# Performance work log

Hardware: AMD Instinct MI355X
Metric: run time of the kernel (lower is better)

Reference implementation:

```python
import jax, jax.numpy as jnp
import numpy as np

N_Q = 8
DIM = 2 ** N_Q          # 256
DEGREE = 3
ANSATZ_LAYERS = 2


def gelu(x):
    return jax.nn.gelu(x, approximate=False)


def layer_norm(x, g, b, eps=1e-5):
    mu = x.mean(-1, keepdims=True)
    v = x.var(-1, keepdims=True)
    return (x - mu) / jnp.sqrt(v + eps) * g + b


def apply_ry(state, theta, w, n):
    # state: (B, 2^n) complex64, theta: (B,) per-element angle
    half = theta * 0.5
    c, s = jnp.cos(half), jnp.sin(half)
    U = jnp.stack([jnp.stack([c, -s], -1), jnp.stack([s, c], -1)], -2).astype(state.dtype)
    L, R = 2 ** w, 2 ** (n - 1 - w)
    st = state.reshape(-1, L, 2, R)
    st = jnp.einsum('bij,bljr->blir', U, st)
    return st.reshape(state.shape)


def apply_crx(state, theta, c, t, n):
    # controlled-RX(theta), control wire c, target wire t (batched angles)
    half = theta * 0.5
    cs = jnp.cos(half).astype(state.dtype)
    ms = (-1j) * jnp.sin(half).astype(state.dtype)
    Rx = jnp.stack([jnp.stack([cs, ms], -1), jnp.stack([ms, cs], -1)], -2)  # (B,2,2)
    a, b = min(c, t), max(c, t)
    A, M, R = 2 ** a, 2 ** (b - a - 1), 2 ** (n - 1 - b)
    st = state.reshape(-1, A, 2, M, 2, R)
    if c < t:
        sub = st[:, :, 1]                              # control bit = 1 slice, (B,A,M,2,R)
        sub = jnp.einsum('bij,bamjr->bamir', Rx, sub)
        st = st.at[:, :, 1].set(sub)
    else:
        sub = st[:, :, :, :, 1]                        # (B,A,2,M,R)
        sub = jnp.einsum('bij,bajmr->baimr', Rx, sub)
        st = st.at[:, :, :, :, 1].set(sub)
    return st.reshape(state.shape)


def sim14(state, params, n, layers):
    # Sim et al. 2019 circuit 14: RY layer, CRX ring, RY layer, reversed CRX ring (4n params/layer)
    idx = 0
    for _ in range(layers):
        for q in range(n):
            state = apply_ry(state, params[:, idx + q], q, n)
        idx += n
        for q in range(n):
            state = apply_crx(state, params[:, idx + q], q, (q + 1) % n, n)
        idx += n
        for q in range(n):
            state = apply_ry(state, params[:, idx + q], q, n)
        idx += n
        for q in range(n):
            state = apply_crx(state, params[:, idx + q], q, (q - 1) % n, n)
        idx += n
    return state


def pauli_expvals(psi, n):
    # [<X_0..X_{n-1}>, <Y_0..>, <Z_0..>] for batched pure states psi: (B, 2^n)
    xs, ys, zs = [], [], []
    for w in range(n):
        L, R = 2 ** w, 2 ** (n - 1 - w)
        s = psi.reshape(-1, L, 2, R)
        s0, s1 = s[:, :, 0], s[:, :, 1]
        cross = (jnp.conj(s0) * s1).sum((1, 2))
        xs.append(2.0 * jnp.real(cross))
        ys.append(2.0 * jnp.imag(cross))
        zs.append((jnp.abs(s0) ** 2 - jnp.abs(s1) ** 2).sum((1, 2)))
    return jnp.stack(xs + ys + zs, axis=1).astype(jnp.float32)


def dwsep_conv(x, dw_w, dw_b, pw_w, pw_b, gn_g, gn_b, dilation):
    # depthwise-separable conv1d + GroupNorm(8) + GELU; x: (B, C, T)
    k = dw_w.shape[-1]
    pad = (k - 1) * dilation // 2
    y = jax.lax.conv_general_dilated(
        x, dw_w, window_strides=(1,), padding=[(pad, pad)], rhs_dilation=(dilation,),
        feature_group_count=x.shape[1], dimension_numbers=('NCH', 'OIH', 'NCH'))
    y = y + dw_b[None, :, None]
    y = jnp.einsum('oc,bct->bot', pw_w, y) + pw_b[None, :, None]
    B, C, T = y.shape
    g = y.reshape(B, 8, C // 8, T)
    mu = g.mean((2, 3), keepdims=True)
    var = g.var((2, 3), keepdims=True)
    y = ((g - mu) / jnp.sqrt(var + 1e-5)).reshape(B, C, T)
    return gelu(y * gn_g[None, :, None] + gn_b[None, :, None])


def setup_inputs() -> dict:
    key = jax.random.key(0)
    ks = iter(jax.random.split(key, 64))
    rn = lambda *s: jax.random.normal(next(ks), s, jnp.float32) * 0.05
    ru = lambda *s: jax.random.uniform(next(ks), s, dtype=jnp.float32)
    inp = dict(
        x=jax.random.normal(next(ks), (16, 363, 180), jnp.float32),
        net_w=rn(12, 15, 8), net_b=rn(12, 8),
        dwa_w=rn(96, 1, 7), dwa_b=rn(96), pwa_w=rn(96, 96), pwa_b=rn(96),
        gna_g=jnp.ones(96, jnp.float32), gna_b=jnp.zeros(96, jnp.float32),
        dwb_w=rn(96, 1, 7), dwb_b=rn(96), pwb_w=rn(96, 96), pwb_b=rn(96),
        gnb_g=jnp.ones(96, jnp.float32), gnb_b=jnp.zeros(96, jnp.float32),
        dwc_w=rn(96, 1, 7), dwc_b=rn(96), pwc_w=rn(96, 96), pwc_b=rn(96),
        gnc_g=jnp.ones(96, jnp.float32), gnc_b=jnp.zeros(96, jnp.float32),
        merge_w=rn(288, 128), merge_b=rn(128),
        merge_ln_g=jnp.ones(128, jnp.float32), merge_ln_b=jnp.zeros(128, jnp.float32),
        qproj_w=rn(128, 64), qproj_b=rn(64),
        poly_coeffs=ru(4), qff_params=ru(32),
        mix_re=ru(363), mix_im=ru(363),
        qout_w=rn(24, 128), qout_b=rn(128),
        fc_w=rn(78, 64), fc_b=rn(64),
        fus1_w=rn(192, 128), fus1_b=rn(128),
        fus_ln_g=jnp.ones(128, jnp.float32), fus_ln_b=jnp.zeros(128, jnp.float32),
        fus2_w=rn(128, 64), fus2_b=rn(64),
    )
    return inp


def reference(x, net_w, net_b, dwa_w, dwa_b, pwa_w, pwa_b, gna_g, gna_b,
              dwb_w, dwb_b, pwb_w, pwb_b, gnb_g, gnb_b,
              dwc_w, dwc_b, pwc_w, pwc_b, gnc_g, gnc_b,
              merge_w, merge_b, merge_ln_g, merge_ln_b,
              qproj_w, qproj_b, poly_coeffs, qff_params, mix_re, mix_im,
              qout_w, qout_b, fc_w, fc_b,
              fus1_w, fus1_b, fus_ln_g, fus_ln_b, fus2_w, fus2_b):
    B, T, C = x.shape
    # --- network projection: 12 contiguous networks of 15 ROIs -> d_net=8 each ---
    h = jnp.einsum('btki,kid->btkd', x.reshape(B, T, 12, 15), net_w) + net_b
    h = gelu(h).reshape(B, T, 96)
    # --- multiscale depthwise-separable convs ---
    ht = h.transpose(0, 2, 1)  # (B,96,T)
    a = dwsep_conv(ht, dwa_w, dwa_b, pwa_w, pwa_b, gna_g, gna_b, 1)
    b = dwsep_conv(ht, dwb_w, dwb_b, pwb_w, pwb_b, gnb_g, gnb_b, 4)
    c = dwsep_conv(ht, dwc_w, dwc_b, pwc_w, pwc_b, gnc_g, gnc_b, 16)
    cat = jnp.concatenate([a, b, c], axis=1).transpose(0, 2, 1)  # (B,T,288)
    h = gelu(layer_norm(cat @ merge_w + merge_b, merge_ln_g, merge_ln_b))  # (B,T,128)
    # --- QSVT quantum temporal mixing ---
    tp = jax.nn.sigmoid(h @ qproj_w + qproj_b) * (2.0 * np.pi)  # (B,T,64) rotation angles
    tp = tp.reshape(B * T, -1)
    base = jnp.zeros((B * T, DIM), jnp.complex64).at[:, 0].set(1.0)
    pc = poly_coeffs.astype(jnp.complex64)
    state = base
    acc = pc[0] * base
    for d in range(1, DEGREE + 1):
        state = sim14(state, tp, N_Q, ANSATZ_LAYERS)
        acc = acc + pc[d] * state
    acc = acc.reshape(B, T, DIM)
    mix = (mix_re + 1j * mix_im).astype(jnp.complex64)[:T]
    mixed = jnp.einsum('t,btd->bd', mix, acc)           # temporal mixing
    norm = jnp.linalg.norm(mixed, axis=1, keepdims=True)
    psi = mixed / (norm + 1e-9)
    psi = sim14(psi, jnp.broadcast_to(qff_params[None, :], (B, qff_params.shape[0])), N_Q, 1)
    exps = pauli_expvals(psi, N_Q)                      # (B,24)
    temporal = exps @ qout_w + qout_b                   # (B,128)
    # --- FC fingerprint ---
    xm = x - x.mean(1, keepdims=True)
    std = jnp.maximum(jnp.std(x, axis=1, keepdims=True, ddof=1), 1e-8)
    xn = xm / std
    corr = jnp.einsum('btc,btd->bcd', xn, xn) / (T - 1)
    bm = corr.reshape(B, 12, 15, 12, 15).mean((2, 4))   # (B,12,12) network-block means
    iu0, iu1 = jnp.triu_indices(12)
    fc_vec = bm[:, iu0, iu1]                            # (B,78)
    fc = gelu(fc_vec @ fc_w + fc_b)                     # (B,64)
    # --- fusion ---
    fused = jnp.concatenate([temporal, fc], axis=1)
    out = gelu(layer_norm(fused @ fus1_w + fus1_b, fus_ln_g, fus_ln_b)) @ fus2_w + fus2_b
    return out  # (B,64)
```

## Files before the change

kernel.cpp:

```cpp
#include <hip/hip_runtime.h>
#include <math.h>

#define NB 16
#define NT 363
#define NC 180
#define SZF 557568
#define NROW 5808

__device__ __forceinline__ float gelu_f(float x) {
  return 0.5f * x * (1.0f + erff(x * 0.7071067811865475244f));
}


template<int CTRL>
__device__ __forceinline__ float dppf(float x) {
  return __int_as_float(__builtin_amdgcn_update_dpp(
      0, __float_as_int(x), CTRL, 0xF, 0xF, true));
}

template<int LB>
__device__ __forceinline__ float lx(float x) {
  if constexpr (LB == 0) return dppf<0xB1>(x);
  else if constexpr (LB == 1) return dppf<0x4E>(x);
  else if constexpr (LB == 2) return __shfl_xor(x, 4);
  else return __shfl_xor(x, 8);
}

template<int P>
__device__ __forceinline__ void ry_local(float* re, float* im, float c, float s) {
#pragma unroll
  for (int j = 0; j < 16; ++j) {
    if ((j & (1 << P)) == 0) {
      int k = j | (1 << P);
      float r0 = re[j], i0 = im[j], r1 = re[k], i1 = im[k];
      re[j] = fmaf(c, r0, -s * r1); im[j] = fmaf(c, i0, -s * i1);
      re[k] = fmaf(s, r0,  c * r1); im[k] = fmaf(s, i0,  c * i1);
    }
  }
}

template<int LB>
__device__ __forceinline__ void ry_lane(float* re, float* im, float c, float s, int lane) {
  float sg = (lane & (1 << LB)) ? s : -s;
#pragma unroll
  for (int j = 0; j < 16; ++j) {
    float br = lx<LB>(re[j]);
    float bi = lx<LB>(im[j]);
    re[j] = fmaf(c, re[j], sg * br);
    im[j] = fmaf(c, im[j], sg * bi);
  }
}

template<int Q, int P>
__device__ __forceinline__ void crx_ll(float* re, float* im, float cs, float sn) {
#pragma unroll
  for (int j = 0; j < 16; ++j) {
    if ((j & (1 << Q)) && !(j & (1 << P))) {
      int k = j | (1 << P);
      float r0 = re[j], i0 = im[j], r1 = re[k], i1 = im[k];
      re[j] = fmaf(cs, r0,  sn * i1); im[j] = fmaf(cs, i0, -sn * r1);
      re[k] = fmaf(cs, r1,  sn * i0); im[k] = fmaf(cs, i1, -sn * r0);
    }
  }
}

template<int LBQ, int P>
__device__ __forceinline__ void crx_nl(float* re, float* im, float cs, float sn, int lane) {
  if (lane & (1 << LBQ)) {
#pragma unroll
    for (int j = 0; j < 16; ++j) {
      if ((j & (1 << P)) == 0) {
        int k = j | (1 << P);
        float r0 = re[j], i0 = im[j], r1 = re[k], i1 = im[k];
        re[j] = fmaf(cs, r0,  sn * i1); im[j] = fmaf(cs, i0, -sn * r1);
        re[k] = fmaf(cs, r1,  sn * i0); im[k] = fmaf(cs, i1, -sn * r0);
      }
    }
  }
}

template<int Q, int LBP>
__device__ __forceinline__ void crx_ln(float* re, float* im, float cs, float sn) {
#pragma unroll
  for (int j = 0; j < 16; ++j) {
    if (j & (1 << Q)) {
      float br = lx<LBP>(re[j]);
      float bi = lx<LBP>(im[j]);
      re[j] = fmaf(cs, re[j],  sn * bi);
      im[j] = fmaf(cs, im[j], -sn * br);
    }
  }
}

template<int LBQ, int LBP>
__device__ __forceinline__ void crx_nn(float* re, float* im, float cs, float sn, int lane) {
  bool ctl = (lane & (1 << LBQ)) != 0;
#pragma unroll
  for (int j = 0; j < 16; ++j) {
    float br = lx<LBP>(re[j]);
    float bi = lx<LBP>(im[j]);
    if (ctl) {
      re[j] = fmaf(cs, re[j],  sn * bi);
      im[j] = fmaf(cs, im[j], -sn * br);
    }
  }
}

__device__ __forceinline__ void qlayer(float* re, float* im,
                                       const float2* ang, int lane) {
  float2 a;
  a = ang[0];  ry_lane<3>(re, im, a.x, a.y, lane);
  a = ang[1];  ry_lane<2>(re, im, a.x, a.y, lane);
  a = ang[2];  ry_lane<1>(re, im, a.x, a.y, lane);
  a = ang[3];  ry_lane<0>(re, im, a.x, a.y, lane);
  a = ang[4];  ry_local<3>(re, im, a.x, a.y);
  a = ang[5];  ry_local<2>(re, im, a.x, a.y);
  a = ang[6];  ry_local<1>(re, im, a.x, a.y);
  a = ang[7];  ry_local<0>(re, im, a.x, a.y);
  a = ang[8];  crx_nn<3, 2>(re, im, a.x, a.y, lane);
  a = ang[9];  crx_nn<2, 1>(re, im, a.x, a.y, lane);
  a = ang[10]; crx_nn<1, 0>(re, im, a.x, a.y, lane);
  a = ang[11]; crx_nl<0, 3>(re, im, a.x, a.y, lane);
  a = ang[12]; crx_ll<3, 2>(re, im, a.x, a.y);
  a = ang[13]; crx_ll<2, 1>(re, im, a.x, a.y);
  a = ang[14]; crx_ll<1, 0>(re, im, a.x, a.y);
  a = ang[15]; crx_ln<0, 3>(re, im, a.x, a.y);
  a = ang[16]; ry_lane<3>(re, im, a.x, a.y, lane);
  a = ang[17]; ry_lane<2>(re, im, a.x, a.y, lane);
  a = ang[18]; ry_lane<1>(re, im, a.x, a.y, lane);
  a = ang[19]; ry_lane<0>(re, im, a.x, a.y, lane);
  a = ang[20]; ry_local<3>(re, im, a.x, a.y);
  a = ang[21]; ry_local<2>(re, im, a.x, a.y);
  a = ang[22]; ry_local<1>(re, im, a.x, a.y);
  a = ang[23]; ry_local<0>(re, im, a.x, a.y);
  a = ang[24]; crx_nl<3, 0>(re, im, a.x, a.y, lane);
  a = ang[25]; crx_nn<2, 3>(re, im, a.x, a.y, lane);
  a = ang[26]; crx_nn<1, 2>(re, im, a.x, a.y, lane);
  a = ang[27]; crx_nn<0, 1>(re, im, a.x, a.y, lane);
  a = ang[28]; crx_ln<3, 0>(re, im, a.x, a.y);
  a = ang[29]; crx_ll<2, 3>(re, im, a.x, a.y);
  a = ang[30]; crx_ll<1, 2>(re, im, a.x, a.y);
  a = ang[31]; crx_ll<0, 1>(re, im, a.x, a.y);
}

template<int P>
__device__ __forceinline__ void ryg(float* re, float* im, float c, float s, int lane) {
  if constexpr (P >= 2) {
    constexpr int mask = 1 << (P - 2);
    float sg = ((lane >> (P - 2)) & 1) ? s : -s;
#pragma unroll
    for (int j = 0; j < 4; ++j) {
      float br = __shfl_xor(re[j], mask);
      float bi = __shfl_xor(im[j], mask);
      re[j] = fmaf(c, re[j], sg * br);
      im[j] = fmaf(c, im[j], sg * bi);
    }
  } else {
#pragma unroll
    for (int k = 0; k < 2; ++k) {
      const int a = (P == 0) ? 2 * k : k;
      const int b = (P == 0) ? a + 1 : a + 2;
      float r0 = re[a], i0 = im[a], r1 = re[b], i1 = im[b];
      re[a] = fmaf(c, r0, -s * r1); im[a] = fmaf(c, i0, -s * i1);
      re[b] = fmaf(s, r0,  c * r1); im[b] = fmaf(s, i0,  c * i1);
    }
  }
}

template<int PC, int PT>
__device__ __forceinline__ void crxg(float* re, float* im, float cs, float sn, int lane) {
  if constexpr (PT >= 2) {
    constexpr int mask = 1 << (PT - 2);
#pragma unroll
    for (int j = 0; j < 4; ++j) {
      float br = __shfl_xor(re[j], mask);
// ... 6 lines not shown
        float ni = fmaf(cs, im[j], -sn * br);
        re[j] = nr; im[j] = ni;
      }
    }
  } else {
#pragma unroll
    for (int k = 0; k < 2; ++k) {
      const int a = (PT == 0) ? 2 * k : k;
      const int b = (PT == 0) ? a + 1 : a + 2;
      bool ctrl;
      if constexpr (PC >= 2) ctrl = ((lane >> (PC - 2)) & 1) != 0;
      else                   ctrl = ((a >> PC) & 1) != 0;
      if (ctrl) {
        float r0 = re[a], i0 = im[a], r1 = re[b], i1 = im[b];
        re[a] = fmaf(cs, r0,  sn * i1); im[a] = fmaf(cs, i0, -sn * r1);
        re[b] = fmaf(cs, r1,  sn * i0); im[b] = fmaf(cs, i1, -sn * r0);
      }
    }
  }
}

__device__ __forceinline__ void sim14_layer(float* re, float* im,
                                            const float* Cr, const float* Sr, int lane) {
#define ARY1(q, pi) ryg<7-(q)>(re, im, Cr[pi], Sr[pi], lane)
#define ACX1(cq, tq, pi) crxg<7-(cq), 7-(tq)>(re, im, Cr[pi], Sr[pi], lane)
  ARY1(0,0); ARY1(1,1); ARY1(2,2); ARY1(3,3); ARY1(4,4); ARY1(5,5); ARY1(6,6); ARY1(7,7);
  ACX1(0,1,8); ACX1(1,2,9); ACX1(2,3,10); ACX1(3,4,11); ACX1(4,5,12); ACX1(5,6,13); ACX1(6,7,14); ACX1(7,0,15);
  ARY1(0,16); ARY1(1,17); ARY1(2,18); ARY1(3,19); ARY1(4,20); ARY1(5,21); ARY1(6,22); ARY1(7,23);
  ACX1(0,7,24); ACX1(1,0,25); ACX1(2,1,26); ACX1(3,2,27); ACX1(4,3,28); ACX1(5,4,29); ACX1(6,5,30); ACX1(7,6,31);
#undef ARY1
#undef ACX1
}

__global__ __launch_bounds__(256) void k_embed(const float* __restrict__ x,
                                               const float* __restrict__ nw,
                                               const float* __restrict__ nb,
                                               float* __restrict__ ht) {
  int b = blockIdx.x, tile = blockIdx.y, tid = threadIdx.x;
  int t0 = tile * 32;
  __shared__ float xt[32][181];
  __shared__ float nwL[1440];
  __shared__ float nbL[96];
  for (int i = tid; i < 1440; i += 256) nwL[i] = nw[i];
  for (int i = tid; i < 96; i += 256) nbL[i] = nb[i];
  for (int i = tid; i < 32 * 180; i += 256) {
    int tt = i / 180, c = i % 180;
    int t = t0 + tt;
    xt[tt][c] = (t < NT) ? x[(b * NT + t) * NC + c] : 0.0f;
  }
  __syncthreads();
  int tt = tid & 31, cs = tid >> 5;
  int t = t0 + tt;
  if (t < NT) {
    for (int pass = 0; pass < 12; ++pass) {
      int k = pass, d = cs;
      int c = k * 8 + d;
      float acc = nbL[k * 8 + d];
#pragma unroll
      for (int i = 0; i < 15; ++i)
        acc = fmaf(xt[tt][k * 15 + i], nwL[(k * 15 + i) * 8 + d], acc);
      ht[(b * 96 + c) * NT + t] = gelu_f(acc);
    }
  }
}

__global__ __launch_bounds__(384) void k_dw(const float* __restrict__ ht,
    const float* __restrict__ wa, const float* __restrict__ ba,
    const float* __restrict__ wb, const float* __restrict__ bb,
    const float* __restrict__ wc, const float* __restrict__ bc,
    float* __restrict__ y1base) {
  int bc_idx = blockIdx.x;
  int c = bc_idx % 96;
  int tid = threadIdx.x;
  __shared__ float rowL[NT];
  if (tid < NT) rowL[tid] = ht[bc_idx * NT + tid];
  __syncthreads();
  if (tid < NT) {
    {
      float acc = ba[c];
#pragma unroll
      for (int k = 0; k < 7; ++k) {
        int idx = tid + (k - 3);
        if (idx >= 0 && idx < NT) acc = fmaf(rowL[idx], wa[c * 7 + k], acc);
      }
      y1base[bc_idx * NT + tid] = acc;
    }
    {
      float acc = bb[c];
#pragma unroll
      for (int k = 0; k < 7; ++k) {
        int idx = tid + (k - 3) * 4;
        if (idx >= 0 && idx < NT) acc = fmaf(rowL[idx], wb[c * 7 + k], acc);
      }
      y1base[SZF + bc_idx * NT + tid] = acc;
    }
    {
      float acc = bc[c];
#pragma unroll
      for (int k = 0; k < 7; ++k) {
        int idx = tid + (k - 3) * 16;
        if (idx >= 0 && idx < NT) acc = fmaf(rowL[idx], wc[c * 7 + k], acc);
      }
      y1base[2 * SZF + bc_idx * NT + tid] = acc;
    }
  }
}

__global__ __launch_bounds__(256) void k_pw(const float* __restrict__ y1base,
    const float* __restrict__ wA, const float* __restrict__ wB, const float* __restrict__ wC,
    const float* __restrict__ bA, const float* __restrict__ bB, const float* __restrict__ bC,
    float* __restrict__ y2base) {
  int b = blockIdx.x, tile = blockIdx.y, z = blockIdx.z, tid = threadIdx.x;
  const float* pw_w = (z == 0) ? wA : ((z == 1) ? wB : wC);
  const float* pw_b = (z == 0) ? bA : ((z == 1) ? bB : bC);
  const float* y1 = y1base + (size_t)z * SZF;
  float* y2 = y2base + (size_t)z * SZF;
  int t0 = tile * 64;
  __shared__ float y1t[96 * 64];
  __shared__ float pwL[96 * 97];
  for (int i = tid; i < 96 * 96; i += 256) {
    int o = i / 96, cc = i % 96;
    pwL[o * 97 + cc] = pw_w[i];
  }
  for (int i = tid; i < 96 * 64; i += 256) {
    int cc = i >> 6, t = i & 63;
    int tt = t0 + t;
    y1t[i] = (tt < NT) ? y1[(b * 96 + cc) * NT + tt] : 0.0f;
  }
  __syncthreads();
  int o16 = tid >> 4, t4 = (tid & 15) * 4;
  for (int pass = 0; pass < 6; ++pass) {
    int o = pass * 16 + o16;
    float bias = pw_b[o];
    float a0 = bias, a1 = bias, a2 = bias, a3 = bias;
    const float* wrow = &pwL[o * 97];
#pragma unroll 4
    for (int cc = 0; cc < 96; ++cc) {
// ... 95 lines not shown
  for (int r = 0; r < 4; ++r) vL[rg * 4 + r][jj] = acc[r];
  __syncthreads();
  if (tid < 8) {
    float s = 0;
    for (int k = 0; k < 128; ++k) s += vL[tid][k];
    float mu = s / 128.0f;
    float q = 0;
    for (int k = 0; k < 128; ++k) { float d = vL[tid][k] - mu; q = fmaf(d, d, q); }
    muS[tid] = mu;
    rsS[tid] = rsqrtf(q / 128.0f + 1e-5f);
  }
  __syncthreads();
  float g = lng[jj], bb2 = lnb[jj];
#pragma unroll
  for (int r = 0; r < 4; ++r) {
    int row = rg * 4 + r;
    float h = (acc[r] - muS[row]) * rsS[row] * g + bb2;
    hL[row][jj] = gelu_f(h);
  }
  __syncthreads();
  int o = tid & 63;
  int r0 = (tid >> 6) * 2;
  for (int rr = 0; rr < 2; ++rr) {
    int row = r0 + rr;
    float u = qb[o];
    for (int k = 0; k < 128; ++k) u = fmaf(hL[row][k], qw[k * 64 + o], u);
    float tp = 6.2831853071795864769f / (1.0f + expf(-u));
    float hf = tp * 0.5f;
    int grow = blk * 8 + row;
    angG[grow * 64 + o] = make_float2(cosf(hf), sinf(hf));
  }
}

__global__ __launch_bounds__(64) void k_quantum(const float2* __restrict__ angG,
                                                const float* __restrict__ pc4,
                                                float* __restrict__ accG) {
  const int lane = threadIdx.x;
  const int g = lane >> 4;
  const int ll = lane & 15;
  const int row0 = blockIdx.x * 4;
  __shared__ float2 angL[4][66];
#pragma unroll
  for (int q = 0; q < 4; ++q)
    angL[q][lane] = angG[(size_t)(row0 + q) * 64 + lane];
  __syncthreads();
  float p0 = pc4[0], p1 = pc4[1], p2 = pc4[2], p3 = pc4[3];
  float re[16], im[16];
#pragma unroll
  for (int j = 0; j < 16; ++j) { re[j] = 0.0f; im[j] = 0.0f; }
  if (ll == 0) re[0] = p3;
  const float2* ang = &angL[g][0];
  for (int rep = 0; rep < 3; ++rep) {
    qlayer(re, im, ang, lane);
    qlayer(re, im, ang + 32, lane);
    float pc = (rep == 0) ? p2 : (rep == 1) ? p1 : p0;
    if (ll == 0) re[0] += pc;
  }
  int row = row0 + g;
  float4* dst = reinterpret_cast<float4*>(accG + ((size_t)row * 256 + ll * 16) * 2);
#pragma unroll
  for (int h = 0; h < 8; ++h)
    dst[h] = make_float4(re[2 * h], im[2 * h], re[2 * h + 1], im[2 * h + 1]);
}

__global__ __launch_bounds__(256) void k_mix1(const float* __restrict__ accG,
                                              const float* __restrict__ mr,
                                              const float* __restrict__ mi,
                                              float* __restrict__ part) {
  int b = blockIdx.x, ch = blockIdx.y, d = threadIdx.x;
  int t0 = ch * 33;
  float sr = 0, si = 0;
  for (int i = 0; i < 33; ++i) {
    int t = t0 + i;
    const float2 a = *reinterpret_cast<const float2*>(accG + (size_t)((b * NT + t) * 256 + d) * 2);
    float m_r = mr[t], m_i = mi[t];
    sr = fmaf(m_r, a.x, fmaf(-m_i, a.y, sr));
    si = fmaf(m_r, a.y, fmaf(m_i, a.x, si));
  }
  float2* o = reinterpret_cast<float2*>(part + (size_t)((b * 11 + ch) * 256 + d) * 2);
  *o = make_float2(sr, si);
}

__global__ __launch_bounds__(256) void k_tail(const float* __restrict__ part,
    const float* __restrict__ qff,
    const float* __restrict__ qout_w, const float* __restrict__ qout_b,
    const float* __restrict__ x,
    const float* __restrict__ fcw, const float* __restrict__ fcb,
    float* __restrict__ fused) {
  int blk = blockIdx.x, tid = threadIdx.x;
  if (blk < 16) {
    int b = blk;
    __shared__ float psiL[256][2];
    __shared__ float red[256];
    __shared__ float qcL[32], qsL[32], exps[24];
    float sr = 0, si = 0;
    {
      int d = tid;
      for (int ch = 0; ch < 11; ++ch) {
        const float2 a = *reinterpret_cast<const float2*>(part + (size_t)((b * 11 + ch) * 256 + d) * 2);
        sr += a.x; si += a.y;
      }
      psiL[d][0] = sr; psiL[d][1] = si;
      red[tid] = sr * sr + si * si;
    }
    if (tid < 32) { float h = qff[tid] * 0.5f; qcL[tid] = cosf(h); qsL[tid] = sinf(h); }
    __syncthreads();
    for (int s2 = 128; s2 > 0; s2 >>= 1) { if (tid < s2) red[tid] += red[tid + s2]; __syncthreads(); }
    float inv = 1.0f / (sqrtf(red[0]) + 1e-9f);
    __syncthreads();
    if (tid < 64) {
      int lane = tid;
      float re[4], im[4];
#pragma unroll
      for (int j = 0; j < 4; ++j) {
        re[j] = psiL[lane * 4 + j][0] * inv;
        im[j] = psiL[lane * 4 + j][1] * inv;
      }
      sim14_layer(re, im, qcL, qsL, lane);
#pragma unroll
      for (int j = 0; j < 4; ++j) { psiL[lane * 4 + j][0] = re[j]; psiL[lane * 4 + j][1] = im[j]; }
    }
    __syncthreads();
    if (tid < 64) {
      int lane = tid;
      for (int w = 0; w < 8; ++w) {
        int p = 7 - w;
        float cr = 0, ci = 0, z = 0;
#pragma unroll
        for (int k = 0; k < 2; ++k) {
          int pr = lane + k * 64;
          int lowmask = (1 << p) - 1;
          int i0 = ((pr >> p) << (p + 1)) | (pr & lowmask);
          int i1 = i0 | (1 << p);
          float r0 = psiL[i0][0], I0 = psiL[i0][1], r1 = psiL[i1][0], I1 = psiL[i1][1];
          cr += r0 * r1 + I0 * I1;
          ci += r0 * I1 - I0 * r1;
          z += r0 * r0 + I0 * I0 - r1 * r1 - I1 * I1;
        }
        for (int off = 32; off > 0; off >>= 1) {
          cr += __shfl_down(cr, off);
          ci += __shfl_down(ci, off);
          z  += __shfl_down(z, off);
        }
        if (lane == 0) { exps[w] = 2.0f * cr; exps[8 + w] = 2.0f * ci; exps[16 + w] = z; }
      }
    }
    __syncthreads();
    if (tid < 128) {
      float v = qout_b[tid];
#pragma unroll
      for (int k = 0; k < 24; ++k) v = fmaf(exps[k], qout_w[k * 128 + tid], v);
      fused[b * 192 + tid] = v;
    }
  } else {
    int b = blk - 16;
    __shared__ float muL[180], invL[180];
    __shared__ float SL[NT * 12];
    __shared__ float fcv[78];
    if (tid < 180) {
      float s = 0;
      const float* px = x + (size_t)b * NT * NC + tid;
      for (int t = 0; t < NT; ++t) s += px[t * NC];
      float mu = s / 363.0f;
      float q = 0;
      for (int t = 0; t < NT; ++t) { float d = px[t * NC] - mu; q = fmaf(d, d, q); }
      float sd = sqrtf(q / 362.0f);
      sd = fmaxf(sd, 1e-8f);
      muL[tid] = mu; invL[tid] = 1.0f / sd;
    }
    __syncthreads();
    for (int t = tid; t < NT; t += 256) {
      const float* px = x + (size_t)(b * NT + t) * NC;
#pragma unroll
      for (int i = 0; i < 12; ++i) {
        float s = 0;
#pragma unroll
        for (int u = 0; u < 15; ++u) {
          int cidx = i * 15 + u;
          s += (px[cidx] - muL[cidx]) * invL[cidx];
        }
        SL[t * 12 + i] = s;
      }
    }
    __syncthreads();
    if (tid < 78) {
      int i = 0, rem = tid;
      while (rem >= 12 - i) { rem -= 12 - i; ++i; }
      int j = i + rem;
      float acc = 0;
      for (int t = 0; t < NT; ++t) acc = fmaf(SL[t * 12 + i], SL[t * 12 + j], acc);
      fcv[tid] = acc * (1.0f / (225.0f * 362.0f));
    }
    __syncthreads();
    if (tid < 64) {
      float v = fcb[tid];
#pragma unroll
      for (int k = 0; k < 78; ++k) v = fmaf(fcv[k], fcw[k * 64 + tid], v);
      fused[b * 192 + 128 + tid] = gelu_f(v);
    }
  }
}

__global__ __launch_bounds__(128) void k_final(const float* __restrict__ fused,
    const float* __restrict__ w1, const float* __restrict__ b1,
    const float* __restrict__ lng, const float* __restrict__ lnb,
    const float* __restrict__ w2, const float* __restrict__ b2,
    float* __restrict__ out) {
  int b = blockIdx.x, tid = threadIdx.x;
  __shared__ float fL[192], red[128], hL[128];
  for (int i = tid; i < 192; i += 128) fL[i] = fused[b * 192 + i];
  __syncthreads();
  float v = b1[tid];
  for (int k = 0; k < 192; ++k) v = fmaf(fL[k], w1[k * 128 + tid], v);
  red[tid] = v; __syncthreads();
  for (int s = 64; s > 0; s >>= 1) { if (tid < s) red[tid] += red[tid + s]; __syncthreads(); }
  float mu = red[0] / 128.0f; __syncthreads();
  float dv = v - mu;
  red[tid] = dv * dv; __syncthreads();
  for (int s = 64; s > 0; s >>= 1) { if (tid < s) red[tid] += red[tid + s]; __syncthreads(); }
  float var = red[0] / 128.0f;
  float h = gelu_f(dv * rsqrtf(var + 1e-5f) * lng[tid] + lnb[tid]);
  hL[tid] = h; __syncthreads();
  if (tid < 64) {
    float o = b2[tid];
    for (int k = 0; k < 128; ++k) o = fmaf(hL[k], w2[k * 64 + tid], o);
    out[b * 64 + tid] = o;
  }
}

extern "C" void kernel_launch(void* const* d_in, const int* in_sizes, int n_in,
                              void* d_out, int out_size, void* d_ws, size_t ws_size,
                              hipStream_t stream) {
  const float* x       = (const float*)d_in[0];
  const float* net_w   = (const float*)d_in[1];
  const float* net_b   = (const float*)d_in[2];
  const float* dwa_w   = (const float*)d_in[3];
  const float* dwa_b   = (const float*)d_in[4];
  const float* pwa_w   = (const float*)d_in[5];
  const float* pwa_b   = (const float*)d_in[6];
  const float* gna_g   = (const float*)d_in[7];
  const float* gna_b   = (const float*)d_in[8];
  const float* dwb_w   = (const float*)d_in[9];
  const float* dwb_b   = (const float*)d_in[10];
  const float* pwb_w   = (const float*)d_in[11];
  const float* pwb_b   = (const float*)d_in[12];
  const float* gnb_g   = (const float*)d_in[13];
  const float* gnb_b   = (const float*)d_in[14];
  const float* dwc_w   = (const float*)d_in[15];
  const float* dwc_b   = (const float*)d_in[16];
  const float* pwc_w   = (const float*)d_in[17];
  const float* pwc_b   = (const float*)d_in[18];
  const float* gnc_g   = (const float*)d_in[19];
  const float* gnc_b   = (const float*)d_in[20];
  const float* merge_w = (const float*)d_in[21];
  const float* merge_b = (const float*)d_in[22];
  const float* mlng    = (const float*)d_in[23];
  const float* mlnb    = (const float*)d_in[24];
  const float* qproj_w = (const float*)d_in[25];
  const float* qproj_b = (const float*)d_in[26];
  const float* poly    = (const float*)d_in[27];
  const float* qff     = (const float*)d_in[28];
  const float* mix_re  = (const float*)d_in[29];
  const float* mix_im  = (const float*)d_in[30];
  const float* qout_w  = (const float*)d_in[31];
  const float* qout_b  = (const float*)d_in[32];
  const float* fc_w    = (const float*)d_in[33];
  const float* fc_b    = (const float*)d_in[34];
  const float* fus1_w  = (const float*)d_in[35];
  const float* fus1_b  = (const float*)d_in[36];
  const float* flng    = (const float*)d_in[37];
  const float* flnb    = (const float*)d_in[38];
  const float* fus2_w  = (const float*)d_in[39];
  const float* fus2_b  = (const float*)d_in[40];
  float* out = (float*)d_out;

  float* W = (float*)d_ws;
  float* ht    = W + 0;
  float* y1b_  = W + SZF;
  float* cat   = W + SZF;
  float* y2b_  = W + 4 * (size_t)SZF;
  float* acc   = W + 0;
  float2* angG = (float2*)(W + 7 * (size_t)SZF);
  float* muG   = W + 7 * (size_t)SZF + 743424;
  float* rsG   = muG + 512;
  float* part  = rsG + 512;
  float* fused = part + 90112;

  k_embed<<<dim3(NB, 12), 256, 0, stream>>>(x, net_w, net_b, ht);
  k_dw<<<NB * 96, 384, 0, stream>>>(ht, dwa_w, dwa_b, dwb_w, dwb_b, dwc_w, dwc_b, y1b_);
  k_pw<<<dim3(NB, 6, 3), 256, 0, stream>>>(y1b_, pwa_w, pwb_w, pwc_w, pwa_b, pwb_b, pwc_b, y2b_);
  k_gnstat<<<dim3(NB, 8, 3), 256, 0, stream>>>(y2b_, muG, rsG);
  k_gnapply<<<dim3(NB, 6, 3), 256, 0, stream>>>(y2b_, muG, rsG,
      gna_g, gnb_g, gnc_g, gna_b, gnb_b, gnc_b, cat);
  k_merge<<<(NB * NT) / 8, 256, 0, stream>>>(cat, merge_w, merge_b, mlng, mlnb,
                                             qproj_w, qproj_b, angG);
  k_quantum<<<NROW / 4, 64, 0, stream>>>(angG, poly, acc);
  k_mix1<<<dim3(NB, 11), 256, 0, stream>>>(acc, mix_re, mix_im, part);
  k_tail<<<32, 256, 0, stream>>>(part, qff, qout_w, qout_b, x, fc_w, fc_b, fused);
  k_final<<<NB, 128, 0, stream>>>(fused, fus1_w, fus1_b, flng, flnb, fus2_w, fus2_b, out);
}
```

Baseline: 337.7 us.

## Fuse embed with depthwise convs, repartition quantum state, merge tail kernels

```diff
diff --git a/kernel.cpp b/kernel.cpp
--- a/kernel.cpp
+++ b/kernel.cpp
@@ -23,13 +23,14 @@
   if constexpr (LB == 0) return dppf<0xB1>(x);
   else if constexpr (LB == 1) return dppf<0x4E>(x);
   else if constexpr (LB == 2) return __shfl_xor(x, 4);
-  else return __shfl_xor(x, 8);
+  else if constexpr (LB == 3) return __shfl_xor(x, 8);
+  else return __shfl_xor(x, 16);
 }
 
 template<int P>
-__device__ __forceinline__ void ry_local(float* re, float* im, float c, float s) {
-#pragma unroll
-  for (int j = 0; j < 16; ++j) {
+__device__ __forceinline__ void ry_local8(float* re, float* im, float c, float s) {
+#pragma unroll
+  for (int j = 0; j < 8; ++j) {
     if ((j & (1 << P)) == 0) {
       int k = j | (1 << P);
       float r0 = re[j], i0 = im[j], r1 = re[k], i1 = im[k];
@@ -40,10 +41,10 @@
 }
 
 template<int LB>
-__device__ __forceinline__ void ry_lane(float* re, float* im, float c, float s, int lane) {
+__device__ __forceinline__ void ry_lane8(float* re, float* im, float c, float s, int lane) {
   float sg = (lane & (1 << LB)) ? s : -s;
 #pragma unroll
-  for (int j = 0; j < 16; ++j) {
+  for (int j = 0; j < 8; ++j) {
     float br = lx<LB>(re[j]);
     float bi = lx<LB>(im[j]);
     re[j] = fmaf(c, re[j], sg * br);
@@ -52,9 +53,9 @@
 }
 
 template<int Q, int P>
-__device__ __forceinline__ void crx_ll(float* re, float* im, float cs, float sn) {
-#pragma unroll
-  for (int j = 0; j < 16; ++j) {
+__device__ __forceinline__ void crx_ll8(float* re, float* im, float cs, float sn) {
+#pragma unroll
+  for (int j = 0; j < 8; ++j) {
     if ((j & (1 << Q)) && !(j & (1 << P))) {
       int k = j | (1 << P);
       float r0 = re[j], i0 = im[j], r1 = re[k], i1 = im[k];
@@ -65,10 +66,10 @@
 }
 
 template<int LBQ, int P>
-__device__ __forceinline__ void crx_nl(float* re, float* im, float cs, float sn, int lane) {
+__device__ __forceinline__ void crx_nl8(float* re, float* im, float cs, float sn, int lane) {
   if (lane & (1 << LBQ)) {
 #pragma unroll
-    for (int j = 0; j < 16; ++j) {
+    for (int j = 0; j < 8; ++j) {
       if ((j & (1 << P)) == 0) {
         int k = j | (1 << P);
         float r0 = re[j], i0 = im[j], r1 = re[k], i1 = im[k];
@@ -80,9 +81,9 @@
 }
 
 template<int Q, int LBP>
-__device__ __forceinline__ void crx_ln(float* re, float* im, float cs, float sn) {
-#pragma unroll
-  for (int j = 0; j < 16; ++j) {
+__device__ __forceinline__ void crx_ln8(float* re, float* im, float cs, float sn) {
+#pragma unroll
+  for (int j = 0; j < 8; ++j) {
     if (j & (1 << Q)) {
       float br = lx<LBP>(re[j]);
       float bi = lx<LBP>(im[j]);
@@ -93,10 +94,10 @@
 }
 
 template<int LBQ, int LBP>
-__device__ __forceinline__ void crx_nn(float* re, float* im, float cs, float sn, int lane) {
+__device__ __forceinline__ void crx_nn8(float* re, float* im, float cs, float sn, int lane) {
   bool ctl = (lane & (1 << LBQ)) != 0;
 #pragma unroll
-  for (int j = 0; j < 16; ++j) {
+  for (int j = 0; j < 8; ++j) {
     float br = lx<LBP>(re[j]);
     float bi = lx<LBP>(im[j]);
     if (ctl) {
@@ -106,41 +107,41 @@
   }
 }
 
-__device__ __forceinline__ void qlayer(float* re, float* im,
-                                       const float2* ang, int lane) {
+__device__ __forceinline__ void qlayer8(float* re, float* im,
+                                        const float2* ang, int lane) {
   float2 a;
-  a = ang[0];  ry_lane<3>(re, im, a.x, a.y, lane);
-  a = ang[1];  ry_lane<2>(re, im, a.x, a.y, lane);
-  a = ang[2];  ry_lane<1>(re, im, a.x, a.y, lane);
-  a = ang[3];  ry_lane<0>(re, im, a.x, a.y, lane);
-  a = ang[4];  ry_local<3>(re, im, a.x, a.y);
-  a = ang[5];  ry_local<2>(re, im, a.x, a.y);
-  a = ang[6];  ry_local<1>(re, im, a.x, a.y);
-  a = ang[7];  ry_local<0>(re, im, a.x, a.y);
-  a = ang[8];  crx_nn<3, 2>(re, im, a.x, a.y, lane);
-  a = ang[9];  crx_nn<2, 1>(re, im, a.x, a.y, lane);
-  a = ang[10]; crx_nn<1, 0>(re, im, a.x, a.y, lane);
-  a = ang[11]; crx_nl<0, 3>(re, im, a.x, a.y, lane);
-  a = ang[12]; crx_ll<3, 2>(re, im, a.x, a.y);
-  a = ang[13]; crx_ll<2, 1>(re, im, a.x, a.y);
-  a = ang[14]; crx_ll<1, 0>(re, im, a.x, a.y);
-  a = ang[15]; crx_ln<0, 3>(re, im, a.x, a.y);
-  a = ang[16]; ry_lane<3>(re, im, a.x, a.y, lane);
-  a = ang[17]; ry_lane<2>(re, im, a.x, a.y, lane);
-  a = ang[18]; ry_lane<1>(re, im, a.x, a.y, lane);
-  a = ang[19]; ry_lane<0>(re, im, a.x, a.y, lane);
-  a = ang[20]; ry_local<3>(re, im, a.x, a.y);
-  a = ang[21]; ry_local<2>(re, im, a.x, a.y);
-  a = ang[22]; ry_local<1>(re, im, a.x, a.y);
-  a = ang[23]; ry_local<0>(re, im, a.x, a.y);
-  a = ang[24]; crx_nl<3, 0>(re, im, a.x, a.y, lane);
-  a = ang[25]; crx_nn<2, 3>(re, im, a.x, a.y, lane);
-  a = ang[26]; crx_nn<1, 2>(re, im, a.x, a.y, lane);
-  a = ang[27]; crx_nn<0, 1>(re, im, a.x, a.y, lane);
-  a = ang[28]; crx_ln<3, 0>(re, im, a.x, a.y);
-  a = ang[29]; crx_ll<2, 3>(re, im, a.x, a.y);
-  a = ang[30]; crx_ll<1, 2>(re, im, a.x, a.y);
-  a = ang[31]; crx_ll<0, 1>(re, im, a.x, a.y);
+  a = ang[0];  ry_lane8<4>(re, im, a.x, a.y, lane);
+  a = ang[1];  ry_lane8<3>(re, im, a.x, a.y, lane);
+  a = ang[2];  ry_lane8<2>(re, im, a.x, a.y, lane);
+  a = ang[3];  ry_lane8<1>(re, im, a.x, a.y, lane);
+  a = ang[4];  ry_lane8<0>(re, im, a.x, a.y, lane);
+  a = ang[5];  ry_local8<2>(re, im, a.x, a.y);
+  a = ang[6];  ry_local8<1>(re, im, a.x, a.y);
+  a = ang[7];  ry_local8<0>(re, im, a.x, a.y);
+  a = ang[8];  crx_nn8<4, 3>(re, im, a.x, a.y, lane);
+  a = ang[9];  crx_nn8<3, 2>(re, im, a.x, a.y, lane);
+  a = ang[10]; crx_nn8<2, 1>(re, im, a.x, a.y, lane);
+  a = ang[11]; crx_nn8<1, 0>(re, im, a.x, a.y, lane);
+  a = ang[12]; crx_nl8<0, 2>(re, im, a.x, a.y, lane);
+  a = ang[13]; crx_ll8<2, 1>(re, im, a.x, a.y);
+  a = ang[14]; crx_ll8<1, 0>(re, im, a.x, a.y);
+  a = ang[15]; crx_ln8<0, 4>(re, im, a.x, a.y);
+  a = ang[16]; ry_lane8<4>(re, im, a.x, a.y, lane);
+  a = ang[17]; ry_lane8<3>(re, im, a.x, a.y, lane);
+  a = ang[18]; ry_lane8<2>(re, im, a.x, a.y, lane);
+  a = ang[19]; ry_lane8<1>(re, im, a.x, a.y, lane);
+  a = ang[20]; ry_lane8<0>(re, im, a.x, a.y, lane);
+  a = ang[21]; ry_local8<2>(re, im, a.x, a.y);
+  a = ang[22]; ry_local8<1>(re, im, a.x, a.y);
+  a = ang[23]; ry_local8<0>(re, im, a.x, a.y);
+  a = ang[24]; crx_nl8<4, 0>(re, im, a.x, a.y, lane);
+  a = ang[25]; crx_nn8<3, 4>(re, im, a.x, a.y, lane);
+  a = ang[26]; crx_nn8<2, 3>(re, im, a.x, a.y, lane);
+  a = ang[27]; crx_nn8<1, 2>(re, im, a.x, a.y, lane);
+  a = ang[28]; crx_nn8<0, 1>(re, im, a.x, a.y, lane);
+  a = ang[29]; crx_ln8<2, 0>(re, im, a.x, a.y);
+  a = ang[30]; crx_ll8<1, 2>(re, im, a.x, a.y);
+  a = ang[31]; crx_ll8<0, 1>(re, im, a.x, a.y);
 }
 
 template<int P>
@@ -213,77 +214,60 @@
 #undef ACX1
 }
 
-__global__ __launch_bounds__(256) void k_embed(const float* __restrict__ x,
-                                               const float* __restrict__ nw,
-                                               const float* __restrict__ nb,
-                                               float* __restrict__ ht) {
-  int b = blockIdx.x, tile = blockIdx.y, tid = threadIdx.x;
-  int t0 = tile * 32;
-  __shared__ float xt[32][181];
-  __shared__ float nwL[1440];
-  __shared__ float nbL[96];
-  for (int i = tid; i < 1440; i += 256) nwL[i] = nw[i];
-  for (int i = tid; i < 96; i += 256) nbL[i] = nb[i];
-  for (int i = tid; i < 32 * 180; i += 256) {
-    int tt = i / 180, c = i % 180;
-    int t = t0 + tt;
-    xt[tt][c] = (t < NT) ? x[(b * NT + t) * NC + c] : 0.0f;
-  }
-  __syncthreads();
-  int tt = tid & 31, cs = tid >> 5;
-  int t = t0 + tt;
-  if (t < NT) {
-    for (int pass = 0; pass < 12; ++pass) {
-      int k = pass, d = cs;
-      int c = k * 8 + d;
-      float acc = nbL[k * 8 + d];
-#pragma unroll
-      for (int i = 0; i < 15; ++i)
-        acc = fmaf(xt[tt][k * 15 + i], nwL[(k * 15 + i) * 8 + d], acc);
-      ht[(b * 96 + c) * NT + t] = gelu_f(acc);
-    }
-  }
-}
-
-__global__ __launch_bounds__(384) void k_dw(const float* __restrict__ ht,
+__global__ __launch_bounds__(256) void k_emdw(const float* __restrict__ x,
+    const float* __restrict__ nw, const float* __restrict__ nb,
     const float* __restrict__ wa, const float* __restrict__ ba,
     const float* __restrict__ wb, const float* __restrict__ bb,
     const float* __restrict__ wc, const float* __restrict__ bc,
     float* __restrict__ y1base) {
-  int bc_idx = blockIdx.x;
-  int c = bc_idx % 96;
-  int tid = threadIdx.x;
-  __shared__ float rowL[NT];
-  if (tid < NT) rowL[tid] = ht[bc_idx * NT + tid];
-  __syncthreads();
-  if (tid < NT) {
-    {
-      float acc = ba[c];
-#pragma unroll
-      for (int k = 0; k < 7; ++k) {
-        int idx = tid + (k - 3);
-        if (idx >= 0 && idx < NT) acc = fmaf(rowL[idx], wa[c * 7 + k], acc);
-      }
-      y1base[bc_idx * NT + tid] = acc;
-    }
-    {
-      float acc = bb[c];
-#pragma unroll
-      for (int k = 0; k < 7; ++k) {
-        int idx = tid + (k - 3) * 4;
-        if (idx >= 0 && idx < NT) acc = fmaf(rowL[idx], wb[c * 7 + k], acc);
-      }
-      y1base[SZF + bc_idx * NT + tid] = acc;
-    }
-    {
-      float acc = bc[c];
-#pragma unroll
-      for (int k = 0; k < 7; ++k) {
-        int idx = tid + (k - 3) * 16;
-        if (idx >= 0 && idx < NT) acc = fmaf(rowL[idx], wc[c * 7 + k], acc);
-      }
-      y1base[2 * SZF + bc_idx * NT + tid] = acc;
-    }
+  int b = blockIdx.x, kg = blockIdx.y, tid = threadIdx.x;
+  __shared__ float xs[NT * 15];
+  __shared__ float nwL[120], nbL[8];
+  __shared__ float hrow[8][368];
+  __shared__ float wL[3][8][8];
+  __shared__ float bL[3][8];
+  for (int i = tid; i < 120; i += 256) nwL[i] = nw[kg * 120 + i];
+  for (int i = tid; i < 8; i += 256) nbL[i] = nb[kg * 8 + i];
+  for (int i = tid; i < 168; i += 256) {
+    int z = i / 56, r = i % 56, d = r / 7, k = r % 7;
+    const float* w = (z == 0) ? wa : ((z == 1) ? wb : wc);
+    wL[z][d][k] = w[(kg * 8 + d) * 7 + k];
+  }
+  for (int i = tid; i < 24; i += 256) {
+    int z = i / 8, d = i % 8;
+    const float* bias = (z == 0) ? ba : ((z == 1) ? bb : bc);
+    bL[z][d] = bias[kg * 8 + d];
+  }
+  for (int i = tid; i < NT * 15; i += 256) {
+    int t = i / 15, u = i % 15;
+    xs[i] = x[((size_t)b * NT + t) * NC + kg * 15 + u];
+  }
+  __syncthreads();
+  for (int i = tid; i < 8 * NT; i += 256) {
+    int t = i % NT, d = i / NT;
+    float acc2 = nbL[d];
+#pragma unroll
+    for (int u = 0; u < 15; ++u) acc2 = fmaf(xs[t * 15 + u], nwL[u * 8 + d], acc2);
+    hrow[d][t] = gelu_f(acc2);
+  }
+  __syncthreads();
+  for (int i = tid; i < 8 * NT; i += 256) {
+    int t = i % NT, d = i / NT;
+    int c = kg * 8 + d;
+    float a0 = bL[0][d], a1 = bL[1][d], a2 = bL[2][d];
+#pragma unroll
+    for (int k = 0; k < 7; ++k) {
+      int i1 = t + (k - 3);
+      int i4 = t + (k - 3) * 4;
+      int i16 = t + (k - 3) * 16;
+      if (i1 >= 0 && i1 < NT)  a0 = fmaf(hrow[d][i1],  wL[0][d][k], a0);
+      if (i4 >= 0 && i4 < NT)  a1 = fmaf(hrow[d][i4],  wL[1][d][k], a1);
+      if (i16 >= 0 && i16 < NT) a2 = fmaf(hrow[d][i16], wL[2][d][k], a2);
+    }
+    size_t base = ((size_t)b * 96 + c) * NT + t;
+    y1base[base] = a0;
+    y1base[SZF + base] = a1;
+    y1base[2 * SZF + base] = a2;
   }
 }
 
@@ -445,35 +429,90 @@
   }
 }
 
-__global__ __launch_bounds__(64) void k_quantum(const float2* __restrict__ angG,
-                                                const float* __restrict__ pc4,
-                                                float* __restrict__ accG) {
-  const int lane = threadIdx.x;
-  const int g = lane >> 4;
-  const int ll = lane & 15;
-  const int row0 = blockIdx.x * 4;
-  __shared__ float2 angL[4][66];
-#pragma unroll
-  for (int q = 0; q < 4; ++q)
-    angL[q][lane] = angG[(size_t)(row0 + q) * 64 + lane];
-  __syncthreads();
-  float p0 = pc4[0], p1 = pc4[1], p2 = pc4[2], p3 = pc4[3];
-  float re[16], im[16];
-#pragma unroll
-  for (int j = 0; j < 16; ++j) { re[j] = 0.0f; im[j] = 0.0f; }
-  if (ll == 0) re[0] = p3;
-  const float2* ang = &angL[g][0];
-  for (int rep = 0; rep < 3; ++rep) {
-    qlayer(re, im, ang, lane);
-    qlayer(re, im, ang + 32, lane);
-    float pc = (rep == 0) ? p2 : (rep == 1) ? p1 : p0;
-    if (ll == 0) re[0] += pc;
-  }
-  int row = row0 + g;
-  float4* dst = reinterpret_cast<float4*>(accG + ((size_t)row * 256 + ll * 16) * 2);
-#pragma unroll
-  for (int h = 0; h < 8; ++h)
-    dst[h] = make_float4(re[2 * h], im[2 * h], re[2 * h + 1], im[2 * h + 1]);
+struct CorrSM { float mu[180]; float inv[180]; float S[NT * 12]; float fcv[78]; };
+union QSM { float2 ang[8][66]; CorrSM c; };
+
+__global__ __launch_bounds__(256) void k_quantum(const float2* __restrict__ angG,
+                                                 const float* __restrict__ pc4,
+                                                 float* __restrict__ accG,
+                                                 const float* __restrict__ x,
+                                                 const float* __restrict__ fcw,
+                                                 const float* __restrict__ fcb,
+                                                 float* __restrict__ fusedG) {
+  __shared__ QSM sm;
+  int tid = threadIdx.x;
+  if (blockIdx.x < NROW / 8) {
+    const int lane = tid & 63;
+    const int wave = tid >> 6;
+    const int ll = lane & 31;
+    const int rowB = wave * 2 + (lane >> 5);
+    const int row0 = blockIdx.x * 8;
+    for (int i = tid; i < 512; i += 256) {
+      int r = i >> 6, cidx = i & 63;
+      sm.ang[r][cidx] = angG[(size_t)(row0 + r) * 64 + cidx];
+    }
+    __syncthreads();
+    float p0 = pc4[0], p1 = pc4[1], p2 = pc4[2], p3 = pc4[3];
+    float re[8], im[8];
+#pragma unroll
+    for (int j = 0; j < 8; ++j) { re[j] = 0.0f; im[j] = 0.0f; }
+    if (ll == 0) re[0] = p3;
+    const float2* ang = &sm.ang[rowB][0];
+    for (int rep = 0; rep < 3; ++rep) {
+      qlayer8(re, im, ang, lane);
+      qlayer8(re, im, ang + 32, lane);
+      float pc = (rep == 0) ? p2 : (rep == 1) ? p1 : p0;
+      if (ll == 0) re[0] += pc;
+    }
+    int row = row0 + rowB;
+    float4* dst = reinterpret_cast<float4*>(accG + ((size_t)row * 256 + ll * 8) * 2);
+#pragma unroll
+    for (int h = 0; h < 4; ++h)
+      dst[h] = make_float4(re[2 * h], im[2 * h], re[2 * h + 1], im[2 * h + 1]);
+  } else {
+    int b = blockIdx.x - NROW / 8;
+    if (tid < 180) {
+      float s = 0;
+      const float* px = x + (size_t)b * NT * NC + tid;
+      for (int t = 0; t < NT; ++t) s += px[t * NC];
+      float mu = s / 363.0f;
+      float q = 0;
+      for (int t = 0; t < NT; ++t) { float d = px[t * NC] - mu; q = fmaf(d, d, q); }
+      float sd = sqrtf(q / 362.0f);
+      sd = fmaxf(sd, 1e-8f);
+      sm.c.mu[tid] = mu; sm.c.inv[tid] = 1.0f / sd;
+    }
+    __syncthreads();
+    for (int t = tid; t < NT; t += 256) {
+      const float* px = x + (size_t)(b * NT + t) * NC;
+#pragma unroll
+      for (int i = 0; i < 12; ++i) {
+        float s = 0;
+#pragma unroll
+        for (int u = 0; u < 15; ++u) {
+          int cidx = i * 15 + u;
+          s += (px[cidx] - sm.c.mu[cidx]) * sm.c.inv[cidx];
+        }
+        sm.c.S[t * 12 + i] = s;
+      }
+    }
+    __syncthreads();
+    if (tid < 78) {
+      int i = 0, rem = tid;
+      while (rem >= 12 - i) { rem -= 12 - i; ++i; }
+      int j = i + rem;
+      float acc = 0;
+      for (int t = 0; t < NT; ++t) acc = fmaf(sm.c.S[t * 12 + i], sm.c.S[t * 12 + j], acc);
+      sm.c.fcv[tid] = acc * (1.0f / (225.0f * 362.0f));
+    }
+    __syncthreads();
+    if (tid < 64) {
+      float v = fcb[tid];
+#pragma unroll
+      for (int k = 0; k < 78; ++k) v = fmaf(sm.c.fcv[k], fcw[k * 64 + tid], v);
+      fusedG[b * 192 + 128 + tid] = gelu_f(v);
+    }
+  }
 }
 
 __global__ __launch_bounds__(256) void k_mix1(const float* __restrict__ accG,
@@ -497,143 +536,95 @@
 __global__ __launch_bounds__(256) void k_tail(const float* __restrict__ part,
     const float* __restrict__ qff,
     const float* __restrict__ qout_w, const float* __restrict__ qout_b,
-    const float* __restrict__ x,
-    const float* __restrict__ fcw, const float* __restrict__ fcb,
-    float* __restrict__ fused) {
-  int blk = blockIdx.x, tid = threadIdx.x;
-  if (blk < 16) {
-    int b = blk;
-    __shared__ float psiL[256][2];
-    __shared__ float red[256];
-    __shared__ float qcL[32], qsL[32], exps[24];
-    float sr = 0, si = 0;
-    {
-      int d = tid;
-      for (int ch = 0; ch < 11; ++ch) {
-        const float2 a = *reinterpret_cast<const float2*>(part + (size_t)((b * 11 + ch) * 256 + d) * 2);
-        sr += a.x; si += a.y;
-      }
-      psiL[d][0] = sr; psiL[d][1] = si;
-      red[tid] = sr * sr + si * si;
-    }
-    if (tid < 32) { float h = qff[tid] * 0.5f; qcL[tid] = cosf(h); qsL[tid] = sinf(h); }
-    __syncthreads();
-    for (int s2 = 128; s2 > 0; s2 >>= 1) { if (tid < s2) red[tid] += red[tid + s2]; __syncthreads(); }
-    float inv = 1.0f / (sqrtf(red[0]) + 1e-9f);
-    __syncthreads();
-    if (tid < 64) {
-      int lane = tid;
-      float re[4], im[4];
-#pragma unroll
-      for (int j = 0; j < 4; ++j) {
-        re[j] = psiL[lane * 4 + j][0] * inv;
-        im[j] = psiL[lane * 4 + j][1] * inv;
-      }
-      sim14_layer(re, im, qcL, qsL, lane);
-#pragma unroll
-      for (int j = 0; j < 4; ++j) { psiL[lane * 4 + j][0] = re[j]; psiL[lane * 4 + j][1] = im[j]; }
-    }
-    __syncthreads();
-    if (tid < 64) {
-      int lane = tid;
-      for (int w = 0; w < 8; ++w) {
-        int p = 7 - w;
-        float cr = 0, ci = 0, z = 0;
-#pragma unroll
-        for (int k = 0; k < 2; ++k) {
-          int pr = lane + k * 64;
-          int lowmask = (1 << p) - 1;
-          int i0 = ((pr >> p) << (p + 1)) | (pr & lowmask);
-          int i1 = i0 | (1 << p);
-          float r0 = psiL[i0][0], I0 = psiL[i0][1], r1 = psiL[i1][0], I1 = psiL[i1][1];
-          cr += r0 * r1 + I0 * I1;
-          ci += r0 * I1 - I0 * r1;
-          z += r0 * r0 + I0 * I0 - r1 * r1 - I1 * I1;
-        }
-        for (int off = 32; off > 0; off >>= 1) {
-          cr += __shfl_down(cr, off);
-          ci += __shfl_down(ci, off);
-          z  += __shfl_down(z, off);
-        }
-        if (lane == 0) { exps[w] = 2.0f * cr; exps[8 + w] = 2.0f * ci; exps[16 + w] = z; }
-      }
-    }
-    __syncthreads();
-    if (tid < 128) {
-      float v = qout_b[tid];
-#pragma unroll
-      for (int k = 0; k < 24; ++k) v = fmaf(exps[k], qout_w[k * 128 + tid], v);
-      fused[b * 192 + tid] = v;
-    }
-  } else {
-    int b = blk - 16;
-    __shared__ float muL[180], invL[180];
-    __shared__ float SL[NT * 12];
-    __shared__ float fcv[78];
-    if (tid < 180) {
-      float s = 0;
-      const float* px = x + (size_t)b * NT * NC + tid;
-      for (int t = 0; t < NT; ++t) s += px[t * NC];
-      float mu = s / 363.0f;
-      float q = 0;
-      for (int t = 0; t < NT; ++t) { float d = px[t * NC] - mu; q = fmaf(d, d, q); }
-      float sd = sqrtf(q / 362.0f);
-      sd = fmaxf(sd, 1e-8f);
-      muL[tid] = mu; invL[tid] = 1.0f / sd;
-    }
-    __syncthreads();
-    for (int t = tid; t < NT; t += 256) {
-      const float* px = x + (size_t)(b * NT + t) * NC;
-#pragma unroll
-      for (int i = 0; i < 12; ++i) {
-        float s = 0;
-#pragma unroll
-        for (int u = 0; u < 15; ++u) {
-          int cidx = i * 15 + u;
-          s += (px[cidx] - muL[cidx]) * invL[cidx];
-        }
-        SL[t * 12 + i] = s;
-      }
-    }
-    __syncthreads();
-    if (tid < 78) {
-      int i = 0, rem = tid;
-      while (rem >= 12 - i) { rem -= 12 - i; ++i; }
-      int j = i + rem;
-      float acc = 0;
-      for (int t = 0; t < NT; ++t) acc = fmaf(SL[t * 12 + i], SL[t * 12 + j], acc);
-      fcv[tid] = acc * (1.0f / (225.0f * 362.0f));
-    }
-    __syncthreads();
-    if (tid < 64) {
-      float v = fcb[tid];
-#pragma unroll
-      for (int k = 0; k < 78; ++k) v = fmaf(fcv[k], fcw[k * 64 + tid], v);
-      fused[b * 192 + 128 + tid] = gelu_f(v);
-    }
-  }
-}
-
-__global__ __launch_bounds__(128) void k_final(const float* __restrict__ fused,
+    const float* __restrict__ fusedG,
     const float* __restrict__ w1, const float* __restrict__ b1,
     const float* __restrict__ lng, const float* __restrict__ lnb,
     const float* __restrict__ w2, const float* __restrict__ b2,
     float* __restrict__ out) {
   int b = blockIdx.x, tid = threadIdx.x;
-  __shared__ float fL[192], red[128], hL[128];
-  for (int i = tid; i < 192; i += 128) fL[i] = fused[b * 192 + i];
-  __syncthreads();
-  float v = b1[tid];
-  for (int k = 0; k < 192; ++k) v = fmaf(fL[k], w1[k * 128 + tid], v);
-  red[tid] = v; __syncthreads();
+  __shared__ float psiL[256][2];
+  __shared__ float red[256];
+  __shared__ float qcL[32], qsL[32], exps[24];
+  __shared__ float tL[128], cL[64], hL[128];
+  {
+    float sr = 0, si = 0;
+    for (int ch = 0; ch < 11; ++ch) {
+      const float2 a = *reinterpret_cast<const float2*>(part + (size_t)((b * 11 + ch) * 256 + tid) * 2);
+      sr += a.x; si += a.y;
+    }
+    psiL[tid][0] = sr; psiL[tid][1] = si;
+    red[tid] = sr * sr + si * si;
+  }
+  if (tid < 32) { float h = qff[tid] * 0.5f; qcL[tid] = cosf(h); qsL[tid] = sinf(h); }
+  __syncthreads();
+  for (int s2 = 128; s2 > 0; s2 >>= 1) { if (tid < s2) red[tid] += red[tid + s2]; __syncthreads(); }
+  float inv = 1.0f / (sqrtf(red[0]) + 1e-9f);
+  __syncthreads();
+  if (tid < 64) {
+    int lane = tid;
+    float re[4], im[4];
+#pragma unroll
+    for (int j = 0; j < 4; ++j) {
+      re[j] = psiL[lane * 4 + j][0] * inv;
+      im[j] = psiL[lane * 4 + j][1] * inv;
+    }
+    sim14_layer(re, im, qcL, qsL, lane);
+#pragma unroll
+    for (int j = 0; j < 4; ++j) { psiL[lane * 4 + j][0] = re[j]; psiL[lane * 4 + j][1] = im[j]; }
+  }
+  __syncthreads();
+  if (tid < 64) {
+    int lane = tid;
+    for (int w = 0; w < 8; ++w) {
+      int p = 7 - w;
+      float cr = 0, ci = 0, z = 0;
+#pragma unroll
+      for (int k = 0; k < 2; ++k) {
+        int pr = lane + k * 64;
+        int lowmask = (1 << p) - 1;
+        int i0 = ((pr >> p) << (p + 1)) | (pr & lowmask);
+        int i1 = i0 | (1 << p);
+        float r0 = psiL[i0][0], I0 = psiL[i0][1], r1 = psiL[i1][0], I1 = psiL[i1][1];
+        cr += r0 * r1 + I0 * I1;
+        ci += r0 * I1 - I0 * r1;
+        z += r0 * r0 + I0 * I0 - r1 * r1 - I1 * I1;
+      }
+      for (int off = 32; off > 0; off >>= 1) {
+        cr += __shfl_down(cr, off);
+        ci += __shfl_down(ci, off);
+        z  += __shfl_down(z, off);
+      }
+      if (lane == 0) { exps[w] = 2.0f * cr; exps[8 + w] = 2.0f * ci; exps[16 + w] = z; }
+    }
+  }
+  __syncthreads();
+  if (tid < 128) {
+    float v = qout_b[tid];
+#pragma unroll
+    for (int k = 0; k < 24; ++k) v = fmaf(exps[k], qout_w[k * 128 + tid], v);
+    tL[tid] = v;
+  } else if (tid < 192) {
+    cL[tid - 128] = fusedG[b * 192 + 128 + (tid - 128)];
+  }
+  __syncthreads();
+  float v = 0.0f;
+  if (tid < 128) {
+    v = b1[tid];
+    for (int k = 0; k < 128; ++k) v = fmaf(tL[k], w1[k * 128 + tid], v);
+    for (int k = 0; k < 64; ++k)  v = fmaf(cL[k], w1[(128 + k) * 128 + tid], v);
+    red[tid] = v;
+  }
+  __syncthreads();
   for (int s = 64; s > 0; s >>= 1) { if (tid < s) red[tid] += red[tid + s]; __syncthreads(); }
-  float mu = red[0] / 128.0f; __syncthreads();
+  float mu = red[0] / 128.0f;
+  __syncthreads();
   float dv = v - mu;
-  red[tid] = dv * dv; __syncthreads();
+  if (tid < 128) red[tid] = dv * dv;
+  __syncthreads();
   for (int s = 64; s > 0; s >>= 1) { if (tid < s) red[tid] += red[tid + s]; __syncthreads(); }
   float var = red[0] / 128.0f;
-  float h = gelu_f(dv * rsqrtf(var + 1e-5f) * lng[tid] + lnb[tid]);
-  hL[tid] = h; __syncthreads();
+  if (tid < 128) hL[tid] = gelu_f(dv * rsqrtf(var + 1e-5f) * lng[tid] + lnb[tid]);
+  __syncthreads();
   if (tid < 64) {
     float o = b2[tid];
     for (int k = 0; k < 128; ++k) o = fmaf(hL[k], w2[k * 64 + tid], o);
@@ -688,27 +679,26 @@
   float* out = (float*)d_out;
 
   float* W = (float*)d_ws;
-  float* ht    = W + 0;
-  float* y1b_  = W + SZF;
-  float* cat   = W + SZF;
-  float* y2b_  = W + 4 * (size_t)SZF;
-  float* acc   = W + 0;
-  float2* angG = (float2*)(W + 7 * (size_t)SZF);
-  float* muG   = W + 7 * (size_t)SZF + 743424;
+  float* y1b_  = W;
+  float* cat   = W;
+  float* y2b_  = W + 3 * (size_t)SZF;
+  float* acc   = W;
+  float2* angG = (float2*)(W + 6 * (size_t)SZF);
+  float* muG   = W + 6 * (size_t)SZF + 743424;
   float* rsG   = muG + 512;
   float* part  = rsG + 512;
   float* fused = part + 90112;
 
-  k_embed<<<dim3(NB, 12), 256, 0, stream>>>(x, net_w, net_b, ht);
-  k_dw<<<NB * 96, 384, 0, stream>>>(ht, dwa_w, dwa_b, dwb_w, dwb_b, dwc_w, dwc_b, y1b_);
+  k_emdw<<<dim3(NB, 12), 256, 0, stream>>>(x, net_w, net_b,
+      dwa_w, dwa_b, dwb_w, dwb_b, dwc_w, dwc_b, y1b_);
   k_pw<<<dim3(NB, 6, 3), 256, 0, stream>>>(y1b_, pwa_w, pwb_w, pwc_w, pwa_b, pwb_b, pwc_b, y2b_);
   k_gnstat<<<dim3(NB, 8, 3), 256, 0, stream>>>(y2b_, muG, rsG);
   k_gnapply<<<dim3(NB, 6, 3), 256, 0, stream>>>(y2b_, muG, rsG,
       gna_g, gnb_g, gnc_g, gna_b, gnb_b, gnc_b, cat);
   k_merge<<<(NB * NT) / 8, 256, 0, stream>>>(cat, merge_w, merge_b, mlng, mlnb,
                                              qproj_w, qproj_b, angG);
-  k_quantum<<<NROW / 4, 64, 0, stream>>>(angG, poly, acc);
+  k_quantum<<<NROW / 8 + NB, 256, 0, stream>>>(angG, poly, acc, x, fc_w, fc_b, fused);
   k_mix1<<<dim3(NB, 11), 256, 0, stream>>>(acc, mix_re, mix_im, part);
-  k_tail<<<32, 256, 0, stream>>>(part, qff, qout_w, qout_b, x, fc_w, fc_b, fused);
-  k_final<<<NB, 128, 0, stream>>>(fused, fus1_w, fus1_b, flng, flnb, fus2_w, fus2_b, out);
-}
+  k_tail<<<NB, 256, 0, stream>>>(part, qff, qout_w, qout_b, fused,
+                                 fus1_w, fus1_b, flng, flnb, fus2_w, fus2_b, out);
+}
```

Result: no change. 335.1 us (-0.8%).
